# Kernel tuning notes

Measured on AMD Instinct MI355X. Metric: run time of the kernel, lower is better.

The kernel has to match this reference:

```python
import jax, jax.numpy as jnp
import numpy as np

B, S, D, H, E, K = 4, 2048, 1024, 4096, 8, 2
CAP_RATIO = 1.05


def setup_inputs() -> dict:
    key = jax.random.key(0)
    k0, k1, k2, k3 = jax.random.split(key, 4)
    x = jax.random.normal(k0, (B, S, D), jnp.float32)
    # router gating weight (xavier-uniform-ish scale)
    Wg = jax.random.normal(k1, (E, D), jnp.float32) * np.float32(np.sqrt(2.0 / (D + E)))
    W1 = jax.random.normal(k2, (E, D, H), jnp.float32) * np.float32(0.02)
    b1 = jnp.zeros((E, H), jnp.float32)
    W2 = jax.random.normal(k3, (E, H, D), jnp.float32) * np.float32(0.02)
    b2 = jnp.zeros((E, D), jnp.float32)
    return {"x": x, "Wg": Wg, "W1": W1, "b1": b1, "W2": W2, "b2": b2}


def reference(x, Wg, W1, b1, W2, b2):
    Bs, Ss, Dd = x.shape
    T = Bs * Ss
    C = int(round(K * T * CAP_RATIO / E))  # static buffer capacity per expert
    xf = x.reshape(T, Dd)

    # --- router (eval mode: no noise) ---
    logits = xf @ Wg.T                       # (T, E)
    gates = jax.nn.softmax(logits, axis=-1)  # (T, E)
    topv, topi = jax.lax.top_k(gates, K)     # (T, K)

    # --- capacity-limited dispatch: FCFS over slot-major (slot, token) order ---
    idx_sm = topi.T.reshape(-1)                              # (K*T,) slot-major expert ids
    oh = jax.nn.one_hot(idx_sm, E, dtype=jnp.int32)          # (K*T, E)
    pos_sm = (jnp.cumsum(oh, axis=0) * oh).sum(-1) - 1       # 0-based rank within expert
    within_sm = pos_sm < C
    pos_sm = jnp.where(within_sm, pos_sm, C)                 # C == out-of-bounds sentinel
    pos = pos_sm.reshape(K, T).T                             # (T, K)
    within = within_sm.reshape(K, T).T                       # (T, K) bool

    # --- combine weights: mask dropped slots, renormalize over active slots ---
    w = topv * within.astype(topv.dtype)
    sums = w.sum(-1, keepdims=True)
    w = jnp.where(sums > 0, w / sums, w)

    # --- scatter tokens into per-expert capacity buffers ---
    e_flat = topi.reshape(-1)                                # (T*K,)
    pos_flat = pos.reshape(-1)                               # (T*K,)
    x_ts = jnp.broadcast_to(xf[:, None, :], (T, K, Dd)).reshape(T * K, Dd)
    expert_in = jnp.zeros((E, C, Dd), x.dtype).at[e_flat, pos_flat].set(x_ts, mode='drop')

    # --- per-expert MLP (grouped GEMM) ---
    h = jax.nn.gelu(jnp.einsum('ecd,edh->ech', expert_in, W1) + b1[:, None, :], approximate=False)
    o = jnp.einsum('ech,ehd->ecd', h, W2) + b2[:, None, :]   # (E, C, D)

    # --- gather back and weighted combine (dropped slots gather 0) ---
    y_ts = o.at[e_flat, pos_flat].get(mode='fill', fill_value=0).reshape(T, K, Dd)
    y = jnp.einsum('tk,tkd->td', w, y_ts)                    # (T, D)

    # --- auxiliary losses ---
    imp = gates.sum(0)                                       # (E,)
    l_imp = (jnp.std(imp) / (imp.mean() + 1e-6)) ** 2
    tpe = (oh * within_sm[:, None].astype(jnp.int32)).sum(0).astype(jnp.float32)
    l_load = (jnp.std(tpe) / (tpe.mean() + 1e-6)) ** 2
    l_aux = 0.5 * (l_imp + l_load)

    return y.reshape(Bs, Ss, Dd), l_aux, l_load
```

## Files before the change

### kernel.cpp

```cpp
#include <hip/hip_runtime.h>
#include <math.h>

typedef short short8v __attribute__((ext_vector_type(8)));
typedef float f32x4 __attribute__((ext_vector_type(4)));
typedef unsigned short ushort4v __attribute__((ext_vector_type(4)));

#define T_TOK 8192
#define DDIM 1024
#define HDIM 4096
#define NE 8
#define CCAP 2150
#define CPAD 2304

__device__ __forceinline__ unsigned short f2bf(float f) {
  union { float f; unsigned u; } a; a.f = f;
  unsigned r = a.u + 0x7fffu + ((a.u >> 16) & 1u);
  return (unsigned short)(r >> 16);
}
__device__ __forceinline__ float bf2f(unsigned short h) {
  union { unsigned u; float f; } a; a.u = ((unsigned)h) << 16;
  return a.f;
}

#define GLOAD_LDS16(gp, lp)                                                   \
  __builtin_amdgcn_global_load_lds(                                           \
      (const __attribute__((address_space(1))) void*)(gp),                    \
      (__attribute__((address_space(3))) void*)(lp), 16, 0, 0)

__device__ __forceinline__ short8v ds_read128(unsigned addr) {
  short8v v;
  asm volatile("ds_read_b128 %0, %1" : "=v"(v) : "v"(addr));
  return v;
}

#define BAR() __builtin_amdgcn_s_barrier()
#define WLGKM0()                                  \
  do {                                            \
    asm volatile("s_waitcnt lgkmcnt(0)");         \
    __builtin_amdgcn_sched_barrier(0);            \
  } while (0)

__global__ __launch_bounds__(256) void router_kernel(
    const float* __restrict__ x, const float* __restrict__ Wg,
    int2* __restrict__ topi, float2* __restrict__ topv,
    float* __restrict__ blkimp) {
  __shared__ float wg[NE * DDIM];
  __shared__ float gsh[4][NE];
  int tid = threadIdx.x;
  for (int i = tid; i < NE * DDIM / 4; i += 256)
    ((float4*)wg)[i] = ((const float4*)Wg)[i];
  __syncthreads();
  int w = tid >> 6, lane = tid & 63;
  int t = blockIdx.x * 4 + w;
  const float* xr = x + (size_t)t * DDIM;
  float p[NE] = {0.f, 0.f, 0.f, 0.f, 0.f, 0.f, 0.f, 0.f};
#pragma unroll
  for (int j = 0; j < 16; ++j) {
    float xv = xr[lane + 64 * j];
#pragma unroll
    for (int e = 0; e < NE; ++e)
      p[e] = fmaf(xv, wg[e * DDIM + lane + 64 * j], p[e]);
  }
#pragma unroll
  for (int e = 0; e < NE; ++e) {
#pragma unroll
    for (int off = 32; off > 0; off >>= 1) p[e] += __shfl_xor(p[e], off, 64);
  }
  float mx = p[0];
#pragma unroll
  for (int e = 1; e < NE; ++e) mx = fmaxf(mx, p[e]);
  float g[NE];
  float s = 0.f;
#pragma unroll
  for (int e = 0; e < NE; ++e) { g[e] = expf(p[e] - mx); s += g[e]; }
  float inv = 1.0f / s;
#pragma unroll
  for (int e = 0; e < NE; ++e) g[e] *= inv;
  int i0 = 0; float v0 = g[0];
#pragma unroll
  for (int e = 1; e < NE; ++e) if (g[e] > v0) { v0 = g[e]; i0 = e; }
  int i1 = -1; float v1 = -1.0f;
#pragma unroll
  for (int e = 0; e < NE; ++e)
    if (e != i0 && g[e] > v1) { v1 = g[e]; i1 = e; }
  if (lane == 0) {
    topi[t] = make_int2(i0, i1);
    topv[t] = make_float2(v0, v1);
#pragma unroll
    for (int e = 0; e < NE; ++e) gsh[w][e] = g[e];
  }
  __syncthreads();
  if (tid < NE)
    blkimp[blockIdx.x * NE + tid] =
        gsh[0][tid] + gsh[1][tid] + gsh[2][tid] + gsh[3][tid];
}

__global__ __launch_bounds__(256) void dispatch_kernel(
    const int2* __restrict__ topi, const float2* __restrict__ topv,
    const float* __restrict__ blkimp, int2* __restrict__ posmj,
    float2* __restrict__ wmaj, float* __restrict__ tail) {
  __shared__ unsigned char eid[2 * T_TOK];
  __shared__ unsigned short possm[2 * T_TOK];
  __shared__ int cnt_sh[NE];
  __shared__ float part[32][NE];
  int tid = threadIdx.x;
  for (int i = tid; i < T_TOK; i += 256) {
    int2 ti = topi[i];
    eid[i] = (unsigned char)ti.x;
    eid[T_TOK + i] = (unsigned char)ti.y;
  }
  __syncthreads();
  if (tid < 64) {
    int lane = tid;
    unsigned long long low = (1ull << lane) - 1ull;
    int c0 = 0, c1 = 0, c2 = 0, c3 = 0, c4 = 0, c5 = 0, c6 = 0, c7 = 0;
    for (int base = 0; base < 2 * T_TOK; base += 64) {
      int e = eid[base + lane];
      unsigned long long m0 = __ballot(e == 0);
      unsigned long long m1 = __ballot(e == 1);
      unsigned long long m2 = __ballot(e == 2);
      unsigned long long m3 = __ballot(e == 3);
      unsigned long long m4 = __ballot(e == 4);
      unsigned long long m5 = __ballot(e == 5);
      unsigned long long m6 = __ballot(e == 6);
      unsigned long long m7 = __ballot(e == 7);
      int rank = 0;
      if (e == 0) rank = c0 + __popcll(m0 & low);
      if (e == 1) rank = c1 + __popcll(m1 & low);
      if (e == 2) rank = c2 + __popcll(m2 & low);
      if (e == 3) rank = c3 + __popcll(m3 & low);
      if (e == 4) rank = c4 + __popcll(m4 & low);
      if (e == 5) rank = c5 + __popcll(m5 & low);
      if (e == 6) rank = c6 + __popcll(m6 & low);
      if (e == 7) rank = c7 + __popcll(m7 & low);
      possm[base + lane] = (unsigned short)((rank < CCAP) ? rank : CCAP);
      c0 += __popcll(m0); c1 += __popcll(m1); c2 += __popcll(m2);
      c3 += __popcll(m3); c4 += __popcll(m4); c5 += __popcll(m5);
      c6 += __popcll(m6); c7 += __popcll(m7);
    }
    if (lane == 0) {
      cnt_sh[0] = c0; cnt_sh[1] = c1; cnt_sh[2] = c2; cnt_sh[3] = c3;
      cnt_sh[4] = c4; cnt_sh[5] = c5; cnt_sh[6] = c6; cnt_sh[7] = c7;
    }
  }
  __syncthreads();
  for (int t = tid; t < T_TOK; t += 256) {
    int p0 = possm[t], p1 = possm[T_TOK + t];
    float2 tv = topv[t];
    float w0 = (p0 < CCAP) ? tv.x : 0.0f;
    float w1 = (p1 < CCAP) ? tv.y : 0.0f;
    float s = w0 + w1;
    if (s > 0.0f) { w0 /= s; w1 /= s; }
    posmj[t] = make_int2(p0, p1);
    wmaj[t] = make_float2(w0, w1);
  }
  {
    int sl = tid >> 3, e8 = tid & 7;
    float s = 0.f;
    for (int b = sl; b < 2048; b += 32) s += blkimp[b * NE + e8];
    part[sl][e8] = s;
  }
  __syncthreads();
  if (tid == 0) {
    float imp[NE], te[NE];
    for (int e = 0; e < NE; ++e) {
      float s = 0.f;
      for (int j = 0; j < 32; ++j) s += part[j][e];
      imp[e] = s;
      int c = cnt_sh[e];
      te[e] = (float)(c < CCAP ? c : CCAP);
    }
    float mi = 0.f, mt = 0.f;
    for (int e = 0; e < NE; ++e) { mi += imp[e]; mt += te[e]; }
    mi *= 0.125f; mt *= 0.125f;
    float vi = 0.f, vt = 0.f;
    for (int e = 0; e < NE; ++e) {
      vi += (imp[e] - mi) * (imp[e] - mi);
      vt += (te[e] - mt) * (te[e] - mt);
    }
    vi *= 0.125f; vt *= 0.125f;
    float ai = sqrtf(vi) / (mi + 1e-6f);
    float at = sqrtf(vt) / (mt + 1e-6f);
    tail[0] = 0.5f * (ai * ai + at * at);
    tail[1] = at * at;
  }
}

__global__ __launch_bounds__(256) void scatter_kernel(
    const float* __restrict__ x, const int2* __restrict__ topi,
    const int2* __restrict__ posmj, unsigned short* __restrict__ ein) {
  int tid = threadIdx.x;
  int gid = blockIdx.x * 4 + (tid >> 6);
  int lane = tid & 63;
  int t = gid >> 1, k = gid & 1;
  int2 pp = posmj[t];
  int p = k ? pp.y : pp.x;
  if (p >= CCAP) return;
  int2 ii = topi[t];
  int e = k ? ii.y : ii.x;
  const float4* src = (const float4*)(x + (size_t)t * DDIM);
  unsigned short* dst = ein + ((size_t)e * CPAD + p) * DDIM;
#pragma unroll
  for (int j = 0; j < 4; ++j) {
    int c = j * 64 + lane;
    float4 v = src[c];
    ushort4v o;
    o.x = f2bf(v.x); o.y = f2bf(v.y); o.z = f2bf(v.z); o.w = f2bf(v.w);
    *(ushort4v*)(dst + (size_t)c * 4) = o;
  }
}

__global__ __launch_bounds__(256) void transpose_cvt_kernel(
    const float* __restrict__ W, unsigned short* __restrict__ WT, int R,
    int Cc) {
  __shared__ unsigned short tile[64][72];
  int rt = R >> 6, ct = Cc >> 6;
  int per_e = rt * ct;
  int e = blockIdx.x / per_e;
  int rem = blockIdx.x % per_e;
  int tr = rem % rt, tc = rem / rt;
  int r0 = tr << 6, c0 = tc << 6;
  const float* We = W + (size_t)e * R * Cc;
  unsigned short* WTe = WT + (size_t)e * R * Cc;
  int tid = threadIdx.x;
  {
    int rl = tid >> 2, cb = (tid & 3) << 4;
    const float* src = We + (size_t)(r0 + rl) * Cc + c0 + cb;
#pragma unroll
    for (int j = 0; j < 16; j += 4) {
      float4 v = *(const float4*)(src + j);
      tile[rl][cb + j + 0] = f2bf(v.x);
      tile[rl][cb + j + 1] = f2bf(v.y);
      tile[rl][cb + j + 2] = f2bf(v.z);
      tile[rl][cb + j + 3] = f2bf(v.w);
    }
  }
  __syncthreads();
  {
    int cl = tid >> 2, rb = (tid & 3) << 4;
    unsigned short* dst = WTe + (size_t)(c0 + cl) * R + r0 + rb;
#pragma unroll
    for (int j = 0; j < 16; j += 4) {
      ushort4v o;
      o.x = tile[rb + j + 0][cl];
      o.y = tile[rb + j + 1][cl];
      o.z = tile[rb + j + 2][cl];
      o.w = tile[rb + j + 3][cl];
      *(ushort4v*)(dst + j) = o;
    }
  }
}

template <bool GELU>
__global__ __launch_bounds__(512, 2) void gemm256_kernel(
    const unsigned short* __restrict__ A, const unsigned short* __restrict__ B,
    const float* __restrict__ bias, unsigned short* __restrict__ Out0,
    unsigned short* __restrict__ Out1, int M, int N, int Kz, int Ksub, int NT,
    int mt, int nt) {
  __shared__ __align__(16) char smem[131072];
  int nwg = gridDim.x;
  int bid = blockIdx.x;
  int swz = (bid & 7) * (nwg >> 3) + (bid >> 3);
  int bm = swz % mt;
  int r = swz / mt;
  int bn = r % nt;
  int r2 = r / nt;
  int e = r2 & 7;
  int ks = r2 >> 3;
  unsigned short* Outp = ks ? Out1 : Out0;
  int koff = ks * Ksub;

  int tid = threadIdx.x;
  int w = tid >> 6, lane = tid & 63;
  int wm = w >> 2, wn = w & 3;
  int fr = lane & 15, g = lane >> 4;
  size_t Kzs = (size_t)Kz;
  const char* Ab = (const char*)(A + ((size_t)e * M + (size_t)bm * 256) * Kzs + koff);
  const char* Bb = (const char*)(B + ((size_t)e * N + (size_t)bn * 256) * Kzs + koff);

  size_t ro0 = (size_t)(w * 16 + fr) * Kzs * 2 + (size_t)g * 16;
  size_t ro1 = ro0 + (size_t)128 * Kzs * 2;
  int ld0 = (w << 10) + lane * 16;
  int ld1 = ((8 + w) << 10) + lane * 16;

  auto stage = [&](const char* gb, int buf, int isB, int kh) {
    int base = (isB << 16) + (buf << 15) + (kh << 14);
    GLOAD_LDS16(gb + ro0 + kh * 64, smem + base + ld0);
    GLOAD_LDS16(gb + ro1 + kh * 64, smem + base + ld1);
  };

  unsigned sbase =
      (unsigned)(unsigned long long)(__attribute__((address_space(3))) char*)smem;
  unsigned l16 = (unsigned)(lane * 16);
  unsigned am = sbase + (unsigned)((wm * 8) << 10) + l16;
  unsigned bnr = sbase + 65536u + (unsigned)((wn * 4) << 10) + l16;

  f32x4 acc[8][4] = {};
  short8v Af[4], Bk[4];

#define MM16(RO)                                                           \
  do {                                                                     \
    __builtin_amdgcn_s_setprio(1);                                         \
    _Pragma("unroll") for (int m_ = 0; m_ < 4; ++m_)                       \
        _Pragma("unroll") for (int n_ = 0; n_ < 4; ++n_)                   \
            acc[RO + m_][n_] = __builtin_amdgcn_mfma_f32_16x16x32_bf16(    \
                Af[m_], Bk[n_], acc[RO + m_][n_], 0, 0, 0);                \
    __builtin_amdgcn_s_setprio(0);                                         \
    __builtin_amdgcn_sched_barrier(0);                                     \
  } while (0)

  stage(Ab, 0, 0, 0); stage(Bb, 0, 1, 0);
  stage(Ab, 0, 0, 1); stage(Bb, 0, 1, 1);
  stage(Ab + 128, 1, 0, 0); stage(Bb + 128, 1, 1, 0);
  asm volatile("s_waitcnt vmcnt(8)");
  BAR();

  for (int t = 0; t < NT; ++t) {
    int c = t & 1, cn = c ^ 1;
    unsigned cb = (unsigned)(c << 15);
    const char* At1 = Ab + (size_t)(t + 1) * 128;
    const char* Bt1 = Bb + (size_t)(t + 1) * 128;
    const char* At2 = Ab + (size_t)(t + 2) * 128;
    const char* Bt2 = Bb + (size_t)(t + 2) * 128;
#pragma unroll
    for (int n = 0; n < 4; ++n) Bk[n] = ds_read128(bnr + cb + (n << 10));
#pragma unroll
    for (int m = 0; m < 4; ++m) Af[m] = ds_read128(am + cb + (m << 10));
    if (t + 1 < NT) stage(At1, cn, 0, 1);
    BAR();
    WLGKM0();
    MM16(0);
    BAR();
#pragma unroll
    for (int m = 0; m < 4; ++m)
      Af[m] = ds_read128(am + cb + ((4 + m) << 10));
    if (t + 1 < NT) stage(Bt1, cn, 1, 1);
    BAR();
    WLGKM0();
    MM16(4);
    if (t + 1 < NT) asm volatile("s_waitcnt vmcnt(8)");
    else            asm volatile("s_waitcnt vmcnt(0)");
    BAR();
#pragma unroll
    for (int n = 0; n < 4; ++n)
      Bk[n] = ds_read128(bnr + cb + 16384u + (n << 10));
#pragma unroll
    for (int m = 0; m < 4; ++m)
      Af[m] = ds_read128(am + cb + 16384u + (m << 10));
    if (t + 2 < NT) stage(At2, c, 0, 0);
    BAR();
    WLGKM0();
    MM16(0);
    BAR();
#pragma unroll
    for (int m = 0; m < 4; ++m)
      Af[m] = ds_read128(am + cb + 16384u + ((4 + m) << 10));
    if (t + 2 < NT) stage(Bt2, c, 1, 0);
    BAR();
    WLGKM0();
    MM16(4);
    if (t + 2 < NT)      asm volatile("s_waitcnt vmcnt(8)");
    else if (t + 1 < NT) asm volatile("s_waitcnt vmcnt(4)");
    else                 asm volatile("s_waitcnt vmcnt(0)");
    BAR();
  }
#undef MM16

  float bv[4];
#pragma unroll
  for (int n = 0; n < 4; ++n)
    bv[n] = (ks == 0)
                ? bias[(size_t)e * N + (size_t)bn * 256 + wn * 64 + n * 16 + fr]
                : 0.0f;
  char* wreg = smem + w * 16384;
#pragma unroll
  for (int m = 0; m < 8; ++m)
#pragma unroll
    for (int n = 0; n < 4; ++n)
#pragma unroll
      for (int j = 0; j < 4; ++j) {
        float v = acc[m][n][j] + bv[n];
        if (GELU) v = 0.5f * v * (1.0f + erff(v * 0.70710678118654752f));
        int rl = m * 16 + g * 4 + j;
        *(unsigned short*)(wreg + rl * 128 + (n * 16 + fr) * 2) = f2bf(v);
      }
  unsigned short* Oe = Outp +
                       ((size_t)e * M + (size_t)bm * 256 + (size_t)wm * 128) * N +
                       (size_t)bn * 256 + (size_t)wn * 64;
#pragma unroll
  for (int pass = 0; pass < 16; ++pass) {
    int rr = pass * 8 + (lane >> 3);
    int ch = lane & 7;
    short8v vv = *(const short8v*)(wreg + rr * 128 + ch * 16);
    *(short8v*)(Oe + (size_t)rr * N + ch * 8) = vv;
  }
}

__global__ __launch_bounds__(256) void gather_kernel(
    const unsigned short* __restrict__ obufA,
    const unsigned short* __restrict__ obufB, const int2* __restrict__ topi,
    const int2* __restrict__ posmj, const float2* __restrict__ wmaj,
    float* __restrict__ y) {
  int tid = threadIdx.x;
  int w = tid >> 6, lane = tid & 63;
  int t = blockIdx.x * 4 + w;
  int2 pp = posmj[t];
  int2 ii = topi[t];
  float2 ww = wmaj[t];
  float* yr = y + (size_t)t * DDIM;
  size_t o0 = ((size_t)ii.x * CPAD + pp.x) * DDIM;
  size_t o1 = ((size_t)ii.y * CPAD + pp.y) * DDIM;
  bool v0 = pp.x < CCAP, v1 = pp.y < CCAP;
#pragma unroll
  for (int j = 0; j < 4; ++j) {
    int c = j * 64 + lane;
    float ax = 0.f, ay = 0.f, az = 0.f, aw = 0.f;
    if (v0) {
      ushort4v a = *(const ushort4v*)(obufA + o0 + (size_t)c * 4);
      ushort4v b = *(const ushort4v*)(obufB + o0 + (size_t)c * 4);
      ax += ww.x * (bf2f(a.x) + bf2f(b.x));
      ay += ww.x * (bf2f(a.y) + bf2f(b.y));
      az += ww.x * (bf2f(a.z) + bf2f(b.z));
      aw += ww.x * (bf2f(a.w) + bf2f(b.w));
    }
    if (v1) {
      ushort4v a = *(const ushort4v*)(obufA + o1 + (size_t)c * 4);
      ushort4v b = *(const ushort4v*)(obufB + o1 + (size_t)c * 4);
      ax += ww.y * (bf2f(a.x) + bf2f(b.x));
      ay += ww.y * (bf2f(a.y) + bf2f(b.y));
      az += ww.y * (bf2f(a.z) + bf2f(b.z));
      aw += ww.y * (bf2f(a.w) + bf2f(b.w));
    }
    ((float4*)yr)[c] = make_float4(ax, ay, az, aw);
  }
}

extern "C" void kernel_launch(void* const* d_in, const int* in_sizes, int n_in,
                              void* d_out, int out_size, void* d_ws,
                              size_t ws_size, hipStream_t stream) {
  (void)in_sizes; (void)n_in; (void)out_size; (void)ws_size;
  const float* x = (const float*)d_in[0];
  const float* Wg = (const float*)d_in[1];
  const float* W1 = (const float*)d_in[2];
  const float* b1 = (const float*)d_in[3];
  const float* W2 = (const float*)d_in[4];
  const float* b2 = (const float*)d_in[5];
  float* out = (float*)d_out;

  char* ws = (char*)d_ws;
  size_t off = 0;
  auto alloc = [&](size_t b) {
    char* p = ws + off;
    off += (b + 255) & ~(size_t)255;
    return p;
  };
  unsigned short* ein = (unsigned short*)alloc((size_t)NE * CPAD * DDIM * 2);
  unsigned short* hbuf = (unsigned short*)alloc((size_t)NE * CPAD * HDIM * 2);
  unsigned short* obuf = (unsigned short*)alloc((size_t)NE * CPAD * DDIM * 2);
  unsigned short* w1t = (unsigned short*)alloc((size_t)NE * HDIM * DDIM * 2);
  unsigned short* w2t = (unsigned short*)alloc((size_t)NE * DDIM * HDIM * 2);
  int2* topi = (int2*)alloc(T_TOK * sizeof(int2));
  float2* topv = (float2*)alloc(T_TOK * sizeof(float2));
  int2* posmj = (int2*)alloc(T_TOK * sizeof(int2));
  float2* wmaj = (float2*)alloc(T_TOK * sizeof(float2));
  float* blkimp = (float*)alloc(2048 * NE * sizeof(float));

  transpose_cvt_kernel<<<NE * (DDIM / 64) * (HDIM / 64), 256, 0, stream>>>(
      W1, w1t, DDIM, HDIM);
  transpose_cvt_kernel<<<NE * (HDIM / 64) * (DDIM / 64), 256, 0, stream>>>(
      W2, w2t, HDIM, DDIM);
  router_kernel<<<T_TOK / 4, 256, 0, stream>>>(x, Wg, topi, topv, blkimp);
  dispatch_kernel<<<1, 256, 0, stream>>>(topi, topv, blkimp, posmj, wmaj,
                                         out + (size_t)T_TOK * DDIM);
  scatter_kernel<<<(2 * T_TOK) / 4, 256, 0, stream>>>(x, topi, posmj, ein);

  gemm256_kernel<true><<<NE * 9 * 16, 512, 0, stream>>>(
      ein, w1t, b1, hbuf, hbuf, CPAD, HDIM, DDIM, DDIM, DDIM / 64, 9, 16);
  gemm256_kernel<false><<<NE * 9 * 4 * 2, 512, 0, stream>>>(
      hbuf, w2t, b2, obuf, ein, CPAD, DDIM, HDIM, HDIM / 2, HDIM / 128, 9, 4);

  gather_kernel<<<T_TOK / 4, 256, 0, stream>>>(obuf, ein, topi, posmj, wmaj,
                                               out);
}
```

Measured before the change: 677.4 us.

## Restructure GEMM main loop into single-barrier double-buffered K-tile pipeline

Replaces the four-phase inner loop, which had a barrier around each 16-MFMA chunk and staggered half-tile prefetch, with a simpler scheme. Each iteration prefetches the whole next K tile into the other buffer, reads all A and B fragments for both K halves into registers, and issues two 32-MFMA blocks separated by partial lgkmcnt waits, with one barrier per tile. The goal is fewer barriers and longer uninterrupted MFMA runs. In exchange it keeps twice as many fragment registers live (Af0/Af1 with 8 entries each), which may hurt occupancy or spill. The prefetch distance also shrinks to one tile and is waited on with vmcnt(0) each iteration, which may expose global load latency.

```diff
diff --git a/kernel.cpp b/kernel.cpp
--- a/kernel.cpp
+++ b/kernel.cpp
@@ -34,11 +34,6 @@
 }
 
 #define BAR() __builtin_amdgcn_s_barrier()
-#define WLGKM0()                                  \
-  do {                                            \
-    asm volatile("s_waitcnt lgkmcnt(0)");         \
-    __builtin_amdgcn_sched_barrier(0);            \
-  } while (0)
 
 __global__ __launch_bounds__(256) void router_kernel(
     const float* __restrict__ x, const float* __restrict__ Wg,
@@ -296,75 +291,53 @@
   unsigned bnr = sbase + 65536u + (unsigned)((wn * 4) << 10) + l16;
 
   f32x4 acc[8][4] = {};
-  short8v Af[4], Bk[4];
-
-#define MM16(RO)                                                           \
+  short8v Af0[8], Af1[8], Bk0[4], Bk1[4];
+
+#define MM32(AF, BK)                                                       \
   do {                                                                     \
     __builtin_amdgcn_s_setprio(1);                                         \
-    _Pragma("unroll") for (int m_ = 0; m_ < 4; ++m_)                       \
+    _Pragma("unroll") for (int m_ = 0; m_ < 8; ++m_)                       \
         _Pragma("unroll") for (int n_ = 0; n_ < 4; ++n_)                   \
-            acc[RO + m_][n_] = __builtin_amdgcn_mfma_f32_16x16x32_bf16(    \
-                Af[m_], Bk[n_], acc[RO + m_][n_], 0, 0, 0);                \
+            acc[m_][n_] = __builtin_amdgcn_mfma_f32_16x16x32_bf16(         \
+                AF[m_], BK[n_], acc[m_][n_], 0, 0, 0);                     \
     __builtin_amdgcn_s_setprio(0);                                         \
     __builtin_amdgcn_sched_barrier(0);                                     \
   } while (0)
 
-  stage(Ab, 0, 0, 0); stage(Bb, 0, 1, 0);
-  stage(Ab, 0, 0, 1); stage(Bb, 0, 1, 1);
-  stage(Ab + 128, 1, 0, 0); stage(Bb + 128, 1, 1, 0);
-  asm volatile("s_waitcnt vmcnt(8)");
+  stage(Ab, 0, 0, 0); stage(Ab, 0, 0, 1);
+  stage(Bb, 0, 1, 0); stage(Bb, 0, 1, 1);
+  asm volatile("s_waitcnt vmcnt(0)");
   BAR();
 
   for (int t = 0; t < NT; ++t) {
     int c = t & 1, cn = c ^ 1;
     unsigned cb = (unsigned)(c << 15);
-    const char* At1 = Ab + (size_t)(t + 1) * 128;
-    const char* Bt1 = Bb + (size_t)(t + 1) * 128;
-    const char* At2 = Ab + (size_t)(t + 2) * 128;
-    const char* Bt2 = Bb + (size_t)(t + 2) * 128;
-#pragma unroll
-    for (int n = 0; n < 4; ++n) Bk[n] = ds_read128(bnr + cb + (n << 10));
-#pragma unroll
-    for (int m = 0; m < 4; ++m) Af[m] = ds_read128(am + cb + (m << 10));
-    if (t + 1 < NT) stage(At1, cn, 0, 1);
+    if (t + 1 < NT) {
+      const char* At1 = Ab + (size_t)(t + 1) * 128;
+      const char* Bt1 = Bb + (size_t)(t + 1) * 128;
+      stage(At1, cn, 0, 0); stage(At1, cn, 0, 1);
+      stage(Bt1, cn, 1, 0); stage(Bt1, cn, 1, 1);
+    }
+#pragma unroll
+    for (int n = 0; n < 4; ++n) Bk0[n] = ds_read128(bnr + cb + (n << 10));
+#pragma unroll
+    for (int m = 0; m < 8; ++m) Af0[m] = ds_read128(am + cb + (m << 10));
+#pragma unroll
+    for (int n = 0; n < 4; ++n)
+      Bk1[n] = ds_read128(bnr + cb + 16384u + (n << 10));
+#pragma unroll
+    for (int m = 0; m < 8; ++m)
+      Af1[m] = ds_read128(am + cb + 16384u + (m << 10));
+    asm volatile("s_waitcnt lgkmcnt(12)");
+    __builtin_amdgcn_sched_barrier(0);
+    MM32(Af0, Bk0);
+    asm volatile("s_waitcnt lgkmcnt(0)");
+    __builtin_amdgcn_sched_barrier(0);
+    MM32(Af1, Bk1);
+    asm volatile("s_waitcnt vmcnt(0)");
     BAR();
-    WLGKM0();
-    MM16(0);
-    BAR();
-#pragma unroll
-    for (int m = 0; m < 4; ++m)
-      Af[m] = ds_read128(am + cb + ((4 + m) << 10));
-    if (t + 1 < NT) stage(Bt1, cn, 1, 1);
-    BAR();
-    WLGKM0();
-    MM16(4);
-    if (t + 1 < NT) asm volatile("s_waitcnt vmcnt(8)");
-    else            asm volatile("s_waitcnt vmcnt(0)");
-    BAR();
-#pragma unroll
-    for (int n = 0; n < 4; ++n)
-      Bk[n] = ds_read128(bnr + cb + 16384u + (n << 10));
-#pragma unroll
-    for (int m = 0; m < 4; ++m)
-      Af[m] = ds_read128(am + cb + 16384u + (m << 10));
-    if (t + 2 < NT) stage(At2, c, 0, 0);
-    BAR();
-    WLGKM0();
-    MM16(0);
-    BAR();
-#pragma unroll
-    for (int m = 0; m < 4; ++m)
-      Af[m] = ds_read128(am + cb + 16384u + ((4 + m) << 10));
-    if (t + 2 < NT) stage(Bt2, c, 1, 0);
-    BAR();
-    WLGKM0();
-    MM16(4);
-    if (t + 2 < NT)      asm volatile("s_waitcnt vmcnt(8)");
-    else if (t + 1 < NT) asm volatile("s_waitcnt vmcnt(4)");
-    else                 asm volatile("s_waitcnt vmcnt(0)");
-    BAR();
-  }
-#undef MM16
+  }
+#undef MM32
 
   float bv[4];
 #pragma unroll
```

Result: slower. 728.2 us (+7.5%).

## Double-buffer MFMA fragments to overlap LDS reads with matrix math

Applied to the files above, without the earlier changes.

Restructures the GEMM main loop to keep two sets of A/B register fragments, so LDS reads for the next sub-step are issued before the MFMAs of the current sub-step. Full lgkmcnt(0) waits are replaced with partial waits and the vmcnt thresholds are adjusted. The aim is to hide LDS latency behind matrix-core work and cut barrier stalls. In exchange it needs more VGPRs and more delicate waitcnt and barrier ordering, which risks lower occupancy or races.

```diff
diff --git a/kernel.cpp b/kernel.cpp
--- a/kernel.cpp
+++ b/kernel.cpp
@@ -34,11 +34,6 @@
 }
 
 #define BAR() __builtin_amdgcn_s_barrier()
-#define WLGKM0()                                  \
-  do {                                            \
-    asm volatile("s_waitcnt lgkmcnt(0)");         \
-    __builtin_amdgcn_sched_barrier(0);            \
-  } while (0)
 
 __global__ __launch_bounds__(256) void router_kernel(
     const float* __restrict__ x, const float* __restrict__ Wg,
@@ -296,15 +291,15 @@
   unsigned bnr = sbase + 65536u + (unsigned)((wn * 4) << 10) + l16;
 
   f32x4 acc[8][4] = {};
-  short8v Af[4], Bk[4];
-
-#define MM16(RO)                                                           \
+  short8v A0v[4], A1v[4], B0v[4], B1v[4];
+
+#define MM(AARR, BARR, RO)                                                 \
   do {                                                                     \
     __builtin_amdgcn_s_setprio(1);                                         \
     _Pragma("unroll") for (int m_ = 0; m_ < 4; ++m_)                       \
         _Pragma("unroll") for (int n_ = 0; n_ < 4; ++n_)                   \
             acc[RO + m_][n_] = __builtin_amdgcn_mfma_f32_16x16x32_bf16(    \
-                Af[m_], Bk[n_], acc[RO + m_][n_], 0, 0, 0);                \
+                AARR[m_], BARR[n_], acc[RO + m_][n_], 0, 0, 0);            \
     __builtin_amdgcn_s_setprio(0);                                         \
     __builtin_amdgcn_sched_barrier(0);                                     \
   } while (0)
@@ -314,57 +309,66 @@
   stage(Ab + 128, 1, 0, 0); stage(Bb + 128, 1, 1, 0);
   asm volatile("s_waitcnt vmcnt(8)");
   BAR();
+#pragma unroll
+  for (int n = 0; n < 4; ++n) B0v[n] = ds_read128(bnr + (n << 10));
+#pragma unroll
+  for (int m = 0; m < 4; ++m) A0v[m] = ds_read128(am + (m << 10));
 
   for (int t = 0; t < NT; ++t) {
     int c = t & 1, cn = c ^ 1;
-    unsigned cb = (unsigned)(c << 15);
+    unsigned cb = (unsigned)(c << 15), cnb = (unsigned)(cn << 15);
     const char* At1 = Ab + (size_t)(t + 1) * 128;
     const char* Bt1 = Bb + (size_t)(t + 1) * 128;
     const char* At2 = Ab + (size_t)(t + 2) * 128;
     const char* Bt2 = Bb + (size_t)(t + 2) * 128;
-#pragma unroll
-    for (int n = 0; n < 4; ++n) Bk[n] = ds_read128(bnr + cb + (n << 10));
-#pragma unroll
-    for (int m = 0; m < 4; ++m) Af[m] = ds_read128(am + cb + (m << 10));
+    BAR();
+#pragma unroll
+    for (int m = 0; m < 4; ++m)
+      A1v[m] = ds_read128(am + cb + ((4 + m) << 10));
     if (t + 1 < NT) stage(At1, cn, 0, 1);
+    asm volatile("s_waitcnt lgkmcnt(4)");
+    __builtin_amdgcn_sched_barrier(0);
+    MM(A0v, B0v, 0);
+    asm volatile("s_waitcnt vmcnt(6)");
     BAR();
-    WLGKM0();
-    MM16(0);
+#pragma unroll
+    for (int n = 0; n < 4; ++n)
+      B1v[n] = ds_read128(bnr + cb + 16384u + (n << 10));
+#pragma unroll
+    for (int m = 0; m < 4; ++m)
+      A0v[m] = ds_read128(am + cb + 16384u + (m << 10));
+    if (t + 1 < NT) stage(Bt1, cn, 1, 1);
+    asm volatile("s_waitcnt lgkmcnt(8)");
+    __builtin_amdgcn_sched_barrier(0);
+    MM(A1v, B0v, 4);
     BAR();
 #pragma unroll
     for (int m = 0; m < 4; ++m)
-      Af[m] = ds_read128(am + cb + ((4 + m) << 10));
-    if (t + 1 < NT) stage(Bt1, cn, 1, 1);
+      A1v[m] = ds_read128(am + cb + 16384u + ((4 + m) << 10));
+    if (t + 2 < NT) stage(At2, c, 0, 0);
+    asm volatile("s_waitcnt lgkmcnt(4)");
+    __builtin_amdgcn_sched_barrier(0);
+    MM(A0v, B1v, 0);
+    asm volatile("s_waitcnt vmcnt(6)");
     BAR();
-    WLGKM0();
-    MM16(4);
-    if (t + 1 < NT) asm volatile("s_waitcnt vmcnt(8)");
-    else            asm volatile("s_waitcnt vmcnt(0)");
-    BAR();
-#pragma unroll
-    for (int n = 0; n < 4; ++n)
-      Bk[n] = ds_read128(bnr + cb + 16384u + (n << 10));
-#pragma unroll
-    for (int m = 0; m < 4; ++m)
-      Af[m] = ds_read128(am + cb + 16384u + (m << 10));
-    if (t + 2 < NT) stage(At2, c, 0, 0);
-    BAR();
-    WLGKM0();
-    MM16(0);
-    BAR();
-#pragma unroll
-    for (int m = 0; m < 4; ++m)
-      Af[m] = ds_read128(am + cb + 16384u + ((4 + m) << 10));
-    if (t + 2 < NT) stage(Bt2, c, 1, 0);
-    BAR();
-    WLGKM0();
-    MM16(4);
-    if (t + 2 < NT)      asm volatile("s_waitcnt vmcnt(8)");
-    else if (t + 1 < NT) asm volatile("s_waitcnt vmcnt(4)");
-    else                 asm volatile("s_waitcnt vmcnt(0)");
-    BAR();
-  }
-#undef MM16
+    if (t + 1 < NT) {
+#pragma unroll
+      for (int n = 0; n < 4; ++n)
+        B0v[n] = ds_read128(bnr + cnb + (n << 10));
+#pragma unroll
+      for (int m = 0; m < 4; ++m)
+        A0v[m] = ds_read128(am + cnb + (m << 10));
+      if (t + 2 < NT) stage(Bt2, c, 1, 0);
+      asm volatile("s_waitcnt lgkmcnt(8)");
+    } else {
+      asm volatile("s_waitcnt lgkmcnt(0)");
+    }
+    __builtin_amdgcn_sched_barrier(0);
+    MM(A1v, B1v, 4);
+  }
+#undef MM
+  asm volatile("s_waitcnt vmcnt(0)");
+  BAR();
 
   float bv[4];
 #pragma unroll
```

Result: no change. 678.8 us (+0.2%).
